# Performance work log

Hardware: AMD Instinct MI355X
Metric: run time of the kernel (lower is better)

Reference implementation:

```python
import jax, jax.numpy as jnp
import numpy as np

N_NODES = 100000
N_EDGES = 1600000
IN_DIM = 300
HID = 128
N_CLASSES = 3
N_ASPECTS = 2048


def setup_inputs() -> dict:
    key = jax.random.key(0)
    ks = jax.random.split(key, 8)
    features = jax.random.normal(ks[0], (N_NODES, IN_DIM), dtype=jnp.float32)
    edge_index = jax.random.randint(ks[1], (2, N_EDGES), 0, N_NODES, dtype=jnp.int64)
    aspect_indices = jax.random.randint(ks[2], (N_ASPECTS,), 0, N_NODES, dtype=jnp.int64)
    W1 = jax.random.normal(ks[3], (IN_DIM, HID), dtype=jnp.float32) * (1.0 / np.sqrt(IN_DIM))
    b1 = jnp.zeros((HID,), dtype=jnp.float32)
    W2 = jax.random.normal(ks[4], (HID, HID), dtype=jnp.float32) * (1.0 / np.sqrt(HID))
    b2 = jnp.zeros((HID,), dtype=jnp.float32)
    Wc = jax.random.normal(ks[5], (HID, N_CLASSES), dtype=jnp.float32) * (1.0 / np.sqrt(HID))
    bc = jnp.zeros((N_CLASSES,), dtype=jnp.float32)
    return {"features": features, "edge_index": edge_index, "aspect_indices": aspect_indices,
            "W1": W1, "b1": b1, "W2": W2, "b2": b2, "Wc": Wc, "bc": bc}


def _gcn_norm(edge_index, num_nodes):
    # PyG GCNConv: add self-loops, symmetric normalization D^-1/2 (A+I) D^-1/2
    loop = jnp.arange(num_nodes, dtype=edge_index.dtype)
    src = jnp.concatenate([edge_index[0], loop])
    dst = jnp.concatenate([edge_index[1], loop])
    deg = jax.ops.segment_sum(jnp.ones_like(dst, dtype=jnp.float32), dst,
                              num_segments=num_nodes)
    deg_inv_sqrt = jnp.where(deg > 0, jax.lax.rsqrt(deg), 0.0)
    norm = deg_inv_sqrt[src] * deg_inv_sqrt[dst]  # [E + N]
    return src, dst, norm


def _gcn_conv(x, src, dst, norm, W, b, num_nodes):
    h = x @ W                            # transform first (dim reduction)
    msg = h[src] * norm[:, None]         # gather + scale  [E+N, HID]
    out = jax.ops.segment_sum(msg, dst, num_segments=num_nodes)  # scatter-add
    return out + b


def reference(features, edge_index, aspect_indices, W1, b1, W2, b2, Wc, bc):
    num_nodes = features.shape[0]
    src, dst, norm = _gcn_norm(edge_index, num_nodes)
    h = _gcn_conv(features, src, dst, norm, W1, b1, num_nodes)
    h = jax.nn.relu(h)
    # dropout(p=0.3) -> identity in eval mode
    h = _gcn_conv(h, src, dst, norm, W2, b2, num_nodes)
    aspect_embeddings = h[aspect_indices]          # [N_ASPECTS, HID]
    logits = aspect_embeddings @ Wc + bc           # [N_ASPECTS, 3]
    return logits
```

## Files before the change

kernel.cpp:

```cpp
#include <hip/hip_runtime.h>

constexpr int NN = 100000;
constexpr int NE = 1600000;
constexpr int IN_DIM = 300;
constexpr int HID = 128;
constexpr int NA = 2048;
constexpr int NF_CAP = 50000;
constexpr int G1_BLOCKS = 391;
constexpr int EDGE_BLOCKS = 3125;

using short8 = __attribute__((ext_vector_type(8))) short;
using f32x4  = __attribute__((ext_vector_type(4))) float;

__device__ inline unsigned short f2bf(float x) {
    unsigned u = __float_as_uint(x);
    unsigned r = u + 0x7FFFu + ((u >> 16) & 1u);
    return (unsigned short)(r >> 16);
}
__device__ inline float bf2f(unsigned short h) {
    return __uint_as_float(((unsigned)h) << 16);
}

__device__ inline void gload_lds16(const void* g, void* l) {
    __builtin_amdgcn_global_load_lds(
        (const __attribute__((address_space(1))) unsigned int*)g,
        (__attribute__((address_space(3))) unsigned int*)l, 16, 0, 0);
}

__global__ void k_flag2(const int* __restrict__ asp, unsigned char* __restrict__ flags2,
                        int* __restrict__ flags1) {
    int i = blockIdx.x * blockDim.x + threadIdx.x;
    if (i < NA) {
        int n = asp[i];
        flags2[n] = 1;
        flags1[n] = 1;
    }
}

__global__ __launch_bounds__(1024) void k_scan2_local(const int* __restrict__ degi,
                                                      const int* __restrict__ flags1,
                                                      int* __restrict__ off,
                                                      int* __restrict__ off2,
                                                      int* __restrict__ blksum,
                                                      int* __restrict__ blksum2,
                                                      float* __restrict__ dis) {
    __shared__ int sh[1024];
    __shared__ int sh2[1024];
    int t = threadIdx.x;
    int base = blockIdx.x * 1024;
    int ok = (base + t < NN);
    int f = ok ? flags1[base + t] : 0;
    int d = ok ? degi[base + t] : 0;
    int v = f ? d : 0;
    if (ok) dis[base + t] = rsqrtf((float)d + 1.0f);
    sh[t] = v;
    sh2[t] = f;
    __syncthreads();
    for (int s = 1; s < 1024; s <<= 1) {
        int a = (t >= s) ? sh[t - s] : 0;
        int a2 = (t >= s) ? sh2[t - s] : 0;
        __syncthreads();
        sh[t] += a;
        sh2[t] += a2;
        __syncthreads();
    }
    if (ok) {
        off[base + t] = sh[t] - v;
        off2[base + t] = sh2[t] - f;
    }
    if (t == 1023) {
        blksum[blockIdx.x] = sh[1023];
        blksum2[blockIdx.x] = sh2[1023];
    }
}

__global__ __launch_bounds__(128) void k_scan2_blk(int* __restrict__ blksum,
                                                   int* __restrict__ blksum2, int nb) {
    __shared__ int sh[128];
    __shared__ int sh2[128];
    int t = threadIdx.x;
    int v = (t < nb) ? blksum[t] : 0;
    int v2 = (t < nb) ? blksum2[t] : 0;
    sh[t] = v;
    sh2[t] = v2;
    __syncthreads();
    for (int s = 1; s < 128; s <<= 1) {
        int a = (t >= s) ? sh[t - s] : 0;
        int a2 = (t >= s) ? sh2[t - s] : 0;
        __syncthreads();
        sh[t] += a;
        sh2[t] += a2;
        __syncthreads();
    }
    if (t < nb) {
        blksum[t] = sh[t] - v;
        blksum2[t] = sh2[t] - v2;
    }
}

__global__ void k_scan2_add(int* __restrict__ off, int* __restrict__ off2,
                            const int* __restrict__ blksum, const int* __restrict__ blksum2,
                            const int* __restrict__ flags1,
                            int* __restrict__ list, int* __restrict__ remap,
                            int* __restrict__ nf) {
    int i = blockIdx.x * blockDim.x + threadIdx.x;
    if (i < NN) {
        off[i] += blksum[i >> 10];
        int o2 = off2[i] + blksum2[i >> 10];
        off2[i] = o2;
        int f = flags1[i];
        if (f && o2 < NF_CAP) {
            list[o2] = i;
            remap[i] = o2;
        }
        if (i == NN - 1) {
            int tot = o2 + f;
            *nf = (tot < NF_CAP) ? tot : NF_CAP;
        }
    }
}

__global__ void k_prepB(const float* __restrict__ B, unsigned short* __restrict__ img,
                        int K, int NT) {
    int i = blockIdx.x * blockDim.x + threadIdx.x;
    if (i >= NT * 4096) return;
    int kt = i >> 12;
    int rem = i & 4095;
    int ct = rem >> 9;
    int s = rem & 511;
    int lg = s >> 7;
    int lr = (s >> 3) & 15;
    int j = s & 7;
    int k = kt * 32 + lg * 8 + j;
    int col = ct * 16 + lr;
    float v = (k < K) ? B[k * 128 + col] : 0.f;
    unsigned short hi = f2bf(v);
    unsigned short lo = f2bf(v - bf2f(hi));
    img[kt * 8192 + ct * 1024 + s] = hi;
    img[kt * 8192 + ct * 1024 + 512 + s] = lo;
}

template <int K, int NT>
__device__ __forceinline__ void gemm_dev(int gbid, const float* __restrict__ A,
        const unsigned short* __restrict__ Bimg,
        float* __restrict__ C, int M, const int* __restrict__ Mptr) {
    __shared__ alignas(16) unsigned short ldsB[2][8192];
    const int Mv = Mptr ? *Mptr : M;
    const int row0 = gbid * 128;
    if (row0 >= Mv) return;
    const int t = threadIdx.x;
    const int w = t >> 6;
    const int l = t & 63;
    const int lr = l & 15;
    const int lg = l >> 4;

    const int r0 = row0 + w * 16 + lr;
    const long a0 = (long)(r0 < Mv ? r0 : Mv - 1) * K + lg * 8;

    f32x4 acc[8];
#pragma unroll
    for (int ct = 0; ct < 8; ++ct) acc[ct] = (f32x4){0.f, 0.f, 0.f, 0.f};

    float4 A0[2], A1[2];

    auto LOADA = [&](float4* buf, int kt) {
        const int k0 = kt * 32 + lg * 8;
        const float* s0 = A + a0 + kt * 32;
        if (k0 + 8 <= K) {
            buf[0] = *(const float4*)(s0);
            buf[1] = *(const float4*)(s0 + 4);
        } else {
            float t0[8];
#pragma unroll
            for (int j = 0; j < 8; ++j) t0[j] = (k0 + j < K) ? s0[j] : 0.f;
            buf[0] = make_float4(t0[0], t0[1], t0[2], t0[3]);
            buf[1] = make_float4(t0[4], t0[5], t0[6], t0[7]);
        }
    };

    auto STAGE_B = [&](int buf, int kt) {
        const char* g = (const char*)Bimg + (long)kt * 16384 + w * 2048 + l * 16;
        gload_lds16(g, &ldsB[buf][w * 1024]);
        gload_lds16(g + 1024, &ldsB[buf][w * 1024 + 512]);
    };

    auto CONV = [&](const float4* buf, short8& h0, short8& e0) {
        float v0[8] = {buf[0].x, buf[0].y, buf[0].z, buf[0].w, buf[1].x, buf[1].y, buf[1].z, buf[1].w};
#pragma unroll
        for (int j = 0; j < 8; ++j) {
            unsigned short hi = f2bf(v0[j]);
            h0[j] = (short)hi;
            e0[j] = (short)f2bf(v0[j] - bf2f(hi));
        }
    };

    auto COMPUTE = [&](const unsigned short* bbuf, short8 ah, short8 al) {
#pragma unroll
        for (int ct = 0; ct < 8; ++ct) {
            const unsigned short* bp = bbuf + ct * 1024 + lg * 128 + lr * 8;
            short8 bh = *(const short8*)(bp);
            short8 bl = *(const short8*)(bp + 512);
            acc[ct] = __builtin_amdgcn_mfma_f32_16x16x32_bf16(ah, bh, acc[ct], 0, 0, 0);
            acc[ct] = __builtin_amdgcn_mfma_f32_16x16x32_bf16(al, bh, acc[ct], 0, 0, 0);
            acc[ct] = __builtin_amdgcn_mfma_f32_16x16x32_bf16(ah, bl, acc[ct], 0, 0, 0);
        }
    };

    LOADA(A0, 0);
    STAGE_B(0, 0);
    __syncthreads();
    for (int kt = 0; kt < NT; kt += 2) {
        if (kt + 1 < NT) {
            LOADA(A1, kt + 1);
            STAGE_B(1, kt + 1);
        }
        {
            short8 h0, e0;
            CONV(A0, h0, e0);
            COMPUTE(ldsB[0], h0, e0);
        }
        __syncthreads();
        if (kt + 1 < NT) {
            if (kt + 2 < NT) {
                LOADA(A0, kt + 2);
                STAGE_B(0, kt + 2);
            }
            short8 h0, e0;
            CONV(A1, h0, e0);
            COMPUTE(ldsB[1], h0, e0);
            __syncthreads();
        }
    }
#pragma unroll
    for (int ct = 0; ct < 8; ++ct)
#pragma unroll
        for (int r = 0; r < 4; ++r) {
            int row = row0 + w * 16 + lg * 4 + r;
            if (row < Mv) C[(long)row * 128 + ct * 16 + lr] = acc[ct][r];
        }
}

__global__ __launch_bounds__(512, 4) void k_fusedA(const float* __restrict__ A,
        const unsigned short* __restrict__ Bimg, float* __restrict__ C,
        const int* __restrict__ src, const int* __restrict__ dst,
        const unsigned char* __restrict__ flags2,
        int* __restrict__ degi, int* __restrict__ flags1) {
    if (blockIdx.x < G1_BLOCKS) {
        gemm_dev<IN_DIM, 10>(blockIdx.x, A, Bimg, C, NN, nullptr);
    } else {
        int e = (blockIdx.x - G1_BLOCKS) * 512 + threadIdx.x;
        if (e < NE) {
            int d = dst[e];
            atomicAdd(&degi[d], 1);
            if (flags2[d]) flags1[src[e]] = 1;
        }
    }
}

__global__ __launch_bounds__(512, 4) void k_fusedB(const float* __restrict__ A,
        const unsigned short* __restrict__ Bimg, float* __restrict__ C,
        const int* __restrict__ src, const int* __restrict__ dst,
        const int* __restrict__ flags1,
        int* __restrict__ off, int* __restrict__ csr) {
    if (blockIdx.x < G1_BLOCKS) {
        gemm_dev<IN_DIM, 10>(blockIdx.x + G1_BLOCKS, A, Bimg, C, NN, nullptr);
    } else {
        int e = (blockIdx.x - G1_BLOCKS) * 512 + threadIdx.x;
        if (e < NE) {
            int d = dst[e];
            if (flags1[d]) {
                int pos = atomicAdd(&off[d], 1);
                csr[pos] = src[e];
            }
        }
    }
}

__global__ __launch_bounds__(512, 4) void k_gemm2(const float* __restrict__ A,
        const unsigned short* __restrict__ Bimg, float* __restrict__ C,
        const int* __restrict__ nf) {
    gemm_dev<HID, 4>(blockIdx.x, A, Bimg, C, 0, nf);
}

__global__ __launch_bounds__(256) void k_gather1(const int* __restrict__ list,
                                                 const int* __restrict__ nf,
                                                 const int* __restrict__ csr,
                                                 const int* __restrict__ offpost,
                                                 const float* __restrict__ dis,
                                                 const float* __restrict__ h1,
                                                 const float* __restrict__ b1,
                                                 float* __restrict__ out) {
    int wave = threadIdx.x >> 6;
    int lane = threadIdx.x & 63;
    int half = lane >> 5;
    int sl = lane & 31;
    int idx = blockIdx.x * 4 + wave;
    if (idx >= *nf) return;
    int n = list[idx];
    int start = (n == 0) ? 0 : offpost[n - 1];
    int end = offpost[n];
    float dn = dis[n];
    float ax = 0.f, ay = 0.f, az = 0.f, aw = 0.f;
    int i = start + half;
    for (; i + 2 < end; i += 4) {
        int s0 = csr[i], s1 = csr[i + 2];
        float w0 = dis[s0], w1 = dis[s1];
        float4 v0 = *(const float4*)&h1[(long)s0 * HID + sl * 4];
        float4 v1 = *(const float4*)&h1[(long)s1 * HID + sl * 4];
        ax += w0 * v0.x + w1 * v1.x;
        ay += w0 * v0.y + w1 * v1.y;
        az += w0 * v0.z + w1 * v1.z;
        aw += w0 * v0.w + w1 * v1.w;
    }
    if (i < end) {
        int s = csr[i];
        float wgt = dis[s];
        float4 v = *(const float4*)&h1[(long)s * HID + sl * 4];
        ax += wgt * v.x;
        ay += wgt * v.y;
        az += wgt * v.z;
        aw += wgt * v.w;
    }
    ax += __shfl_xor(ax, 32);
    ay += __shfl_xor(ay, 32);
    az += __shfl_xor(az, 32);
    aw += __shfl_xor(aw, 32);
    if (half == 0) {
        float4 hv = *(const float4*)&h1[(long)n * HID + sl * 4];
        float4 bv = *(const float4*)&b1[sl * 4];
        float4 r;
        r.x = fmaxf(dn * (ax + dn * hv.x) + bv.x, 0.f);
        r.y = fmaxf(dn * (ay + dn * hv.y) + bv.y, 0.f);
        r.z = fmaxf(dn * (az + dn * hv.z) + bv.z, 0.f);
        r.w = fmaxf(dn * (aw + dn * hv.w) + bv.w, 0.f);
        *reinterpret_cast<float4*>(&out[(long)idx * HID + sl * 4]) = r;
    }
}

__global__ __launch_bounds__(256) void k_gather2(const int* __restrict__ asp,
                                                 const int* __restrict__ remap,
                                                 const int* __restrict__ csr,
                                                 const int* __restrict__ offpost,
                                                 const float* __restrict__ dis,
                                                 const float* __restrict__ t2,
                                                 const float* __restrict__ b2,
                                                 const float* __restrict__ Wc,
                                                 const float* __restrict__ bc,
                                                 float* __restrict__ out) {
    int wave = threadIdx.x >> 6;
    int lane = threadIdx.x & 63;
    int a = blockIdx.x * 4 + wave;
    if (a >= NA) return;
    int n = asp[a];
    int start = (n == 0) ? 0 : offpost[n - 1];
    int end = offpost[n];
    float dn = dis[n];
    float ax = 0.f, ay = 0.f;
    int i = start;
    for (; i + 4 <= end; i += 4) {
        int s0 = csr[i], s1 = csr[i + 1], s2 = csr[i + 2], s3 = csr[i + 3];
        float w0 = dis[s0], w1 = dis[s1], w2 = dis[s2], w3 = dis[s3];
        int r0 = remap[s0], r1 = remap[s1], r2 = remap[s2], r3 = remap[s3];
        float2 v0 = *(const float2*)&t2[(long)r0 * HID + lane * 2];
        float2 v1 = *(const float2*)&t2[(long)r1 * HID + lane * 2];
        float2 v2 = *(const float2*)&t2[(long)r2 * HID + lane * 2];
        float2 v3 = *(const float2*)&t2[(long)r3 * HID + lane * 2];
        ax += w0 * v0.x + w1 * v1.x + w2 * v2.x + w3 * v3.x;
        ay += w0 * v0.y + w1 * v1.y + w2 * v2.y + w3 * v3.y;
    }
    for (; i < end; ++i) {
        int s = csr[i];
        float w = dis[s];
        float2 v = *(const float2*)&t2[(long)remap[s] * HID + lane * 2];
        ax += w * v.x;
        ay += w * v.y;
    }
    float2 hv = *(const float2*)&t2[(long)remap[n] * HID + lane * 2];
    float vx = dn * (ax + dn * hv.x) + b2[2 * lane];
    float vy = dn * (ay + dn * hv.y) + b2[2 * lane + 1];
    float l0 = vx * Wc[(2 * lane) * 3 + 0] + vy * Wc[(2 * lane + 1) * 3 + 0];
    float l1 = vx * Wc[(2 * lane) * 3 + 1] + vy * Wc[(2 * lane + 1) * 3 + 1];
    float l2 = vx * Wc[(2 * lane) * 3 + 2] + vy * Wc[(2 * lane + 1) * 3 + 2];
#pragma unroll
    for (int s = 32; s > 0; s >>= 1) {
        l0 += __shfl_xor(l0, s);
        l1 += __shfl_xor(l1, s);
        l2 += __shfl_xor(l2, s);
    }
    if (lane == 0) {
        out[a * 3 + 0] = l0 + bc[0];
        out[a * 3 + 1] = l1 + bc[1];
        out[a * 3 + 2] = l2 + bc[2];
    }
}

extern "C" void kernel_launch(void* const* d_in, const int* in_sizes, int n_in,
                              void* d_out, int out_size, void* d_ws, size_t ws_size,
                              hipStream_t stream) {
    const float* features = (const float*)d_in[0];
    const int* ei = (const int*)d_in[1];
    const int* src = ei;
    const int* dst = ei + NE;
    const int* asp = (const int*)d_in[2];
    const float* W1 = (const float*)d_in[3];
    const float* b1 = (const float*)d_in[4];
    const float* W2 = (const float*)d_in[5];
    const float* b2 = (const float*)d_in[6];
    const float* Wc = (const float*)d_in[7];
    const float* bc = (const float*)d_in[8];
    float* out = (float*)d_out;

    char* ws = (char*)d_ws;
    float* dis   = (float*)(ws + 0);
    unsigned short* bimg1 = (unsigned short*)(ws + 400384);
    unsigned short* bimg2 = (unsigned short*)(ws + 400384 + 163840);
    int*   off   = (int*)  (ws + 800768);
    int*   blksum  = (int*)(ws + 1201152);
    int*   blksum2 = (int*)(ws + 1202176);
    int*   nf    = (int*)  (ws + 1203200);
    int*   csr   = (int*)  (ws + 1203328);
    int*   flags1= (int*)  (ws + 7603328);
    int*   off2  = (int*)  (ws + 8003328);
    int*   list  = (int*)  (ws + 8403328);
    int*   remap = (int*)  (ws + 8803328);
    float* bufA  = (float*)(ws + 9203328);
    float* bufB  = (float*)(ws + 60403328);
    int*   degi  = (int*)  (ws + 60403328);
    unsigned char* flags2 = (unsigned char*)(ws + 86003328);

    const int NB = (NN + 1023) / 1024;

    hipMemsetAsync(degi, 0, NN * sizeof(int), stream);
    hipMemsetAsync(flags1, 0, NN * sizeof(int), stream);
    hipMemsetAsync(flags2, 0, NN, stream);
    k_flag2<<<(NA + 255) / 256, 256, 0, stream>>>(asp, flags2, flags1);
    k_prepB<<<(10 * 4096 + 255) / 256, 256, 0, stream>>>(W1, bimg1, IN_DIM, 10);
    k_prepB<<<(4 * 4096 + 255) / 256, 256, 0, stream>>>(W2, bimg2, HID, 4);

    k_fusedA<<<G1_BLOCKS + EDGE_BLOCKS, 512, 0, stream>>>(
        features, bimg1, bufA, src, dst, flags2, degi, flags1);

    k_scan2_local<<<NB, 1024, 0, stream>>>(degi, flags1, off, off2, blksum, blksum2, dis);
    k_scan2_blk<<<1, 128, 0, stream>>>(blksum, blksum2, NB);
    k_scan2_add<<<(NN + 255) / 256, 256, 0, stream>>>(off, off2, blksum, blksum2,
                                                      flags1, list, remap, nf);

    k_fusedB<<<G1_BLOCKS + EDGE_BLOCKS, 512, 0, stream>>>(
        features, bimg1, bufA, src, dst, flags1, off, csr);

    k_gather1<<<(NF_CAP + 3) / 4, 256, 0, stream>>>(list, nf, csr, off, dis, bufA, b1, bufB);

    k_gemm2<<<(NF_CAP + 127) / 128, 512, 0, stream>>>(bufB, bimg2, bufA, nf);
    k_gather2<<<(NA + 3) / 4, 256, 0, stream>>>(asp, remap, csr, off, dis, bufA, b2, Wc, bc, out);
}
```

Before: 199.6 us.

## Stage B in two large phases and privatize degree counters across eight copies

The GEMM now loads half (or all) of the B image into LDS in one phase instead of double-buffering one k-tile at a time. This removes the per-tile barriers but uses much more LDS, which may lower occupancy. Separately, degree counting now spreads atomics over eight private copies selected by block index, and the scan sums them, to reduce atomic contention. The cost is a larger memset and eight reads per node in the scan.

```diff
diff --git a/kernel.cpp b/kernel.cpp
--- a/kernel.cpp
+++ b/kernel.cpp
@@ -37,7 +37,7 @@
     }
 }
 
-__global__ __launch_bounds__(1024) void k_scan2_local(const int* __restrict__ degi,
+__global__ __launch_bounds__(1024) void k_scan2_local(const int* __restrict__ degi8,
                                                       const int* __restrict__ flags1,
                                                       int* __restrict__ off,
                                                       int* __restrict__ off2,
@@ -50,9 +50,13 @@
     int base = blockIdx.x * 1024;
     int ok = (base + t < NN);
     int f = ok ? flags1[base + t] : 0;
-    int d = ok ? degi[base + t] : 0;
+    int d = 0;
+    if (ok) {
+#pragma unroll
+        for (int j = 0; j < 8; ++j) d += degi8[j * NN + base + t];
+        dis[base + t] = rsqrtf((float)d + 1.0f);
+    }
     int v = f ? d : 0;
-    if (ok) dis[base + t] = rsqrtf((float)d + 1.0f);
     sh[t] = v;
     sh2[t] = f;
     __syncthreads();
@@ -140,11 +144,11 @@
     img[kt * 8192 + ct * 1024 + 512 + s] = lo;
 }
 
-template <int K, int NT>
+template <int K, int NT, int HALF>
 __device__ __forceinline__ void gemm_dev(int gbid, const float* __restrict__ A,
         const unsigned short* __restrict__ Bimg,
         float* __restrict__ C, int M, const int* __restrict__ Mptr) {
-    __shared__ alignas(16) unsigned short ldsB[2][8192];
+    __shared__ alignas(16) unsigned short ldsB[HALF * 8192];
     const int Mv = Mptr ? *Mptr : M;
     const int row0 = gbid * 128;
     if (row0 >= Mv) return;
@@ -178,10 +182,13 @@
         }
     };
 
-    auto STAGE_B = [&](int buf, int kt) {
-        const char* g = (const char*)Bimg + (long)kt * 16384 + w * 2048 + l * 16;
-        gload_lds16(g, &ldsB[buf][w * 1024]);
-        gload_lds16(g + 1024, &ldsB[buf][w * 1024 + 512]);
+    auto STAGE_PH = [&](int ph) {
+#pragma unroll
+        for (int h = 0; h < HALF; ++h) {
+            const char* g = (const char*)Bimg + (long)(ph * HALF + h) * 16384 + w * 2048 + l * 16;
+            gload_lds16(g, &ldsB[h * 8192 + w * 1024]);
+            gload_lds16(g + 1024, &ldsB[h * 8192 + w * 1024 + 512]);
+        }
     };
 
     auto CONV = [&](const float4* buf, short8& h0, short8& e0) {
@@ -206,29 +213,25 @@
         }
     };
 
+    STAGE_PH(0);
     LOADA(A0, 0);
-    STAGE_B(0, 0);
     __syncthreads();
-    for (int kt = 0; kt < NT; kt += 2) {
+#pragma unroll
+    for (int kt = 0; kt < NT; ++kt) {
+        if (HALF < NT && kt == HALF) {
+            __syncthreads();
+            STAGE_PH(1);
+            __syncthreads();
+        }
         if (kt + 1 < NT) {
-            LOADA(A1, kt + 1);
-            STAGE_B(1, kt + 1);
+            if ((kt & 1) == 0) LOADA(A1, kt + 1);
+            else               LOADA(A0, kt + 1);
         }
         {
             short8 h0, e0;
-            CONV(A0, h0, e0);
-            COMPUTE(ldsB[0], h0, e0);
-        }
-        __syncthreads();
-        if (kt + 1 < NT) {
-            if (kt + 2 < NT) {
-                LOADA(A0, kt + 2);
-                STAGE_B(0, kt + 2);
-            }
-            short8 h0, e0;
-            CONV(A1, h0, e0);
-            COMPUTE(ldsB[1], h0, e0);
-            __syncthreads();
+            if ((kt & 1) == 0) { CONV(A0, h0, e0); }
+            else               { CONV(A1, h0, e0); }
+            COMPUTE(&ldsB[(kt % HALF) * 8192], h0, e0);
         }
     }
 #pragma unroll
@@ -244,14 +247,14 @@
         const unsigned short* __restrict__ Bimg, float* __restrict__ C,
         const int* __restrict__ src, const int* __restrict__ dst,
         const unsigned char* __restrict__ flags2,
-        int* __restrict__ degi, int* __restrict__ flags1) {
+        int* __restrict__ degi8, int* __restrict__ flags1) {
     if (blockIdx.x < G1_BLOCKS) {
-        gemm_dev<IN_DIM, 10>(blockIdx.x, A, Bimg, C, NN, nullptr);
+        gemm_dev<IN_DIM, 10, 5>(blockIdx.x, A, Bimg, C, NN, nullptr);
     } else {
         int e = (blockIdx.x - G1_BLOCKS) * 512 + threadIdx.x;
         if (e < NE) {
             int d = dst[e];
-            atomicAdd(&degi[d], 1);
+            atomicAdd(&degi8[(blockIdx.x & 7) * NN + d], 1);
             if (flags2[d]) flags1[src[e]] = 1;
         }
     }
@@ -263,7 +266,7 @@
         const int* __restrict__ flags1,
         int* __restrict__ off, int* __restrict__ csr) {
     if (blockIdx.x < G1_BLOCKS) {
-        gemm_dev<IN_DIM, 10>(blockIdx.x + G1_BLOCKS, A, Bimg, C, NN, nullptr);
+        gemm_dev<IN_DIM, 10, 5>(blockIdx.x + G1_BLOCKS, A, Bimg, C, NN, nullptr);
     } else {
         int e = (blockIdx.x - G1_BLOCKS) * 512 + threadIdx.x;
         if (e < NE) {
@@ -279,7 +282,7 @@
 __global__ __launch_bounds__(512, 4) void k_gemm2(const float* __restrict__ A,
         const unsigned short* __restrict__ Bimg, float* __restrict__ C,
         const int* __restrict__ nf) {
-    gemm_dev<HID, 4>(blockIdx.x, A, Bimg, C, 0, nf);
+    gemm_dev<HID, 4, 4>(blockIdx.x, A, Bimg, C, 0, nf);
 }
 
 __global__ __launch_bounds__(256) void k_gather1(const int* __restrict__ list,
@@ -425,12 +428,12 @@
     int*   remap = (int*)  (ws + 8803328);
     float* bufA  = (float*)(ws + 9203328);
     float* bufB  = (float*)(ws + 60403328);
-    int*   degi  = (int*)  (ws + 60403328);
+    int*   degi8 = (int*)  (ws + 60403328);
     unsigned char* flags2 = (unsigned char*)(ws + 86003328);
 
     const int NB = (NN + 1023) / 1024;
 
-    hipMemsetAsync(degi, 0, NN * sizeof(int), stream);
+    hipMemsetAsync(degi8, 0, 8 * NN * sizeof(int), stream);
     hipMemsetAsync(flags1, 0, NN * sizeof(int), stream);
     hipMemsetAsync(flags2, 0, NN, stream);
     k_flag2<<<(NA + 255) / 256, 256, 0, stream>>>(asp, flags2, flags1);
@@ -438,9 +441,9 @@
     k_prepB<<<(4 * 4096 + 255) / 256, 256, 0, stream>>>(W2, bimg2, HID, 4);
 
     k_fusedA<<<G1_BLOCKS + EDGE_BLOCKS, 512, 0, stream>>>(
-        features, bimg1, bufA, src, dst, flags2, degi, flags1);
-
-    k_scan2_local<<<NB, 1024, 0, stream>>>(degi, flags1, off, off2, blksum, blksum2, dis);
+        features, bimg1, bufA, src, dst, flags2, degi8, flags1);
+
+    k_scan2_local<<<NB, 1024, 0, stream>>>(degi8, flags1, off, off2, blksum, blksum2, dis);
     k_scan2_blk<<<1, 128, 0, stream>>>(blksum, blksum2, NB);
     k_scan2_add<<<(NN + 255) / 256, 256, 0, stream>>>(off, off2, blksum, blksum2,
                                                       flags1, list, remap, nf);
```

Measured after the change: 201.7 us. Within noise of the previous version (+1.1%).

## Halve GEMM row tile with 2x4 wave split and replicate degree counters

Applied to the files above, without the earlier changes.

The GEMM tile shrinks from 128 to 64 rows per block. The 8 waves are split into 4 row groups by 2 column halves, so each wave holds 4 accumulator tiles instead of 8. This doubles the GEMM block count and allows occupancy 8 in launch bounds. Degree atomics are also spread over 8 replicated counter arrays, chosen by block index, to reduce atomic contention; the scan kernel sums them. The cost is more redundant B staging per block, more A-load overhead per row, and a larger memset for the counters.

```diff
diff --git a/kernel.cpp b/kernel.cpp
--- a/kernel.cpp
+++ b/kernel.cpp
@@ -6,7 +6,9 @@
 constexpr int HID = 128;
 constexpr int NA = 2048;
 constexpr int NF_CAP = 50000;
-constexpr int G1_BLOCKS = 391;
+constexpr int G1T = 1563;
+constexpr int G1A = 782;
+constexpr int G1B = G1T - G1A;
 constexpr int EDGE_BLOCKS = 3125;
 
 using short8 = __attribute__((ext_vector_type(8))) short;
@@ -37,7 +39,7 @@
     }
 }
 
-__global__ __launch_bounds__(1024) void k_scan2_local(const int* __restrict__ degi,
+__global__ __launch_bounds__(1024) void k_scan2_local(const int* __restrict__ degi8,
                                                       const int* __restrict__ flags1,
                                                       int* __restrict__ off,
                                                       int* __restrict__ off2,
@@ -50,9 +52,13 @@
     int base = blockIdx.x * 1024;
     int ok = (base + t < NN);
     int f = ok ? flags1[base + t] : 0;
-    int d = ok ? degi[base + t] : 0;
+    int d = 0;
+    if (ok) {
+#pragma unroll
+        for (int j = 0; j < 8; ++j) d += degi8[j * NN + base + t];
+        dis[base + t] = rsqrtf((float)d + 1.0f);
+    }
     int v = f ? d : 0;
-    if (ok) dis[base + t] = rsqrtf((float)d + 1.0f);
     sh[t] = v;
     sh2[t] = f;
     __syncthreads();
@@ -146,20 +152,22 @@
         float* __restrict__ C, int M, const int* __restrict__ Mptr) {
     __shared__ alignas(16) unsigned short ldsB[2][8192];
     const int Mv = Mptr ? *Mptr : M;
-    const int row0 = gbid * 128;
+    const int row0 = gbid * 64;
     if (row0 >= Mv) return;
     const int t = threadIdx.x;
     const int w = t >> 6;
     const int l = t & 63;
     const int lr = l & 15;
     const int lg = l >> 4;
-
-    const int r0 = row0 + w * 16 + lr;
+    const int wr = w & 3;
+    const int wc = w >> 2;
+
+    const int r0 = row0 + wr * 16 + lr;
     const long a0 = (long)(r0 < Mv ? r0 : Mv - 1) * K + lg * 8;
 
-    f32x4 acc[8];
-#pragma unroll
-    for (int ct = 0; ct < 8; ++ct) acc[ct] = (f32x4){0.f, 0.f, 0.f, 0.f};
+    f32x4 acc[4];
+#pragma unroll
+    for (int ct = 0; ct < 4; ++ct) acc[ct] = (f32x4){0.f, 0.f, 0.f, 0.f};
 
     float4 A0[2], A1[2];
 
@@ -196,8 +204,8 @@
 
     auto COMPUTE = [&](const unsigned short* bbuf, short8 ah, short8 al) {
 #pragma unroll
-        for (int ct = 0; ct < 8; ++ct) {
-            const unsigned short* bp = bbuf + ct * 1024 + lg * 128 + lr * 8;
+        for (int ct = 0; ct < 4; ++ct) {
+            const unsigned short* bp = bbuf + (wc * 4 + ct) * 1024 + lg * 128 + lr * 8;
             short8 bh = *(const short8*)(bp);
             short8 bl = *(const short8*)(bp + 512);
             acc[ct] = __builtin_amdgcn_mfma_f32_16x16x32_bf16(ah, bh, acc[ct], 0, 0, 0);
@@ -232,40 +240,40 @@
         }
     }
 #pragma unroll
-    for (int ct = 0; ct < 8; ++ct)
+    for (int ct = 0; ct < 4; ++ct)
 #pragma unroll
         for (int r = 0; r < 4; ++r) {
-            int row = row0 + w * 16 + lg * 4 + r;
-            if (row < Mv) C[(long)row * 128 + ct * 16 + lr] = acc[ct][r];
-        }
-}
-
-__global__ __launch_bounds__(512, 4) void k_fusedA(const float* __restrict__ A,
+            int row = row0 + wr * 16 + lg * 4 + r;
+            if (row < Mv) C[(long)row * 128 + wc * 64 + ct * 16 + lr] = acc[ct][r];
+        }
+}
+
+__global__ __launch_bounds__(512, 8) void k_fusedA(const float* __restrict__ A,
         const unsigned short* __restrict__ Bimg, float* __restrict__ C,
         const int* __restrict__ src, const int* __restrict__ dst,
         const unsigned char* __restrict__ flags2,
-        int* __restrict__ degi, int* __restrict__ flags1) {
-    if (blockIdx.x < G1_BLOCKS) {
+        int* __restrict__ degi8, int* __restrict__ flags1) {
+    if (blockIdx.x < G1A) {
         gemm_dev<IN_DIM, 10>(blockIdx.x, A, Bimg, C, NN, nullptr);
     } else {
-        int e = (blockIdx.x - G1_BLOCKS) * 512 + threadIdx.x;
+        int e = (blockIdx.x - G1A) * 512 + threadIdx.x;
         if (e < NE) {
             int d = dst[e];
-            atomicAdd(&degi[d], 1);
+            atomicAdd(&degi8[(blockIdx.x & 7) * NN + d], 1);
             if (flags2[d]) flags1[src[e]] = 1;
         }
     }
 }
 
-__global__ __launch_bounds__(512, 4) void k_fusedB(const float* __restrict__ A,
+__global__ __launch_bounds__(512, 8) void k_fusedB(const float* __restrict__ A,
         const unsigned short* __restrict__ Bimg, float* __restrict__ C,
         const int* __restrict__ src, const int* __restrict__ dst,
         const int* __restrict__ flags1,
         int* __restrict__ off, int* __restrict__ csr) {
-    if (blockIdx.x < G1_BLOCKS) {
-        gemm_dev<IN_DIM, 10>(blockIdx.x + G1_BLOCKS, A, Bimg, C, NN, nullptr);
+    if (blockIdx.x < G1B) {
+        gemm_dev<IN_DIM, 10>(blockIdx.x + G1A, A, Bimg, C, NN, nullptr);
     } else {
-        int e = (blockIdx.x - G1_BLOCKS) * 512 + threadIdx.x;
+        int e = (blockIdx.x - G1B) * 512 + threadIdx.x;
         if (e < NE) {
             int d = dst[e];
             if (flags1[d]) {
@@ -276,7 +284,7 @@
     }
 }
 
-__global__ __launch_bounds__(512, 4) void k_gemm2(const float* __restrict__ A,
+__global__ __launch_bounds__(512, 8) void k_gemm2(const float* __restrict__ A,
         const unsigned short* __restrict__ Bimg, float* __restrict__ C,
         const int* __restrict__ nf) {
     gemm_dev<HID, 4>(blockIdx.x, A, Bimg, C, 0, nf);
@@ -425,31 +433,31 @@
     int*   remap = (int*)  (ws + 8803328);
     float* bufA  = (float*)(ws + 9203328);
     float* bufB  = (float*)(ws + 60403328);
-    int*   degi  = (int*)  (ws + 60403328);
+    int*   degi8 = (int*)  (ws + 60403328);
     unsigned char* flags2 = (unsigned char*)(ws + 86003328);
 
     const int NB = (NN + 1023) / 1024;
 
-    hipMemsetAsync(degi, 0, NN * sizeof(int), stream);
+    hipMemsetAsync(degi8, 0, 8 * NN * sizeof(int), stream);
     hipMemsetAsync(flags1, 0, NN * sizeof(int), stream);
     hipMemsetAsync(flags2, 0, NN, stream);
     k_flag2<<<(NA + 255) / 256, 256, 0, stream>>>(asp, flags2, flags1);
     k_prepB<<<(10 * 4096 + 255) / 256, 256, 0, stream>>>(W1, bimg1, IN_DIM, 10);
     k_prepB<<<(4 * 4096 + 255) / 256, 256, 0, stream>>>(W2, bimg2, HID, 4);
 
-    k_fusedA<<<G1_BLOCKS + EDGE_BLOCKS, 512, 0, stream>>>(
-        features, bimg1, bufA, src, dst, flags2, degi, flags1);
-
-    k_scan2_local<<<NB, 1024, 0, stream>>>(degi, flags1, off, off2, blksum, blksum2, dis);
+    k_fusedA<<<G1A + EDGE_BLOCKS, 512, 0, stream>>>(
+        features, bimg1, bufA, src, dst, flags2, degi8, flags1);
+
+    k_scan2_local<<<NB, 1024, 0, stream>>>(degi8, flags1, off, off2, blksum, blksum2, dis);
     k_scan2_blk<<<1, 128, 0, stream>>>(blksum, blksum2, NB);
     k_scan2_add<<<(NN + 255) / 256, 256, 0, stream>>>(off, off2, blksum, blksum2,
                                                       flags1, list, remap, nf);
 
-    k_fusedB<<<G1_BLOCKS + EDGE_BLOCKS, 512, 0, stream>>>(
+    k_fusedB<<<G1B + EDGE_BLOCKS, 512, 0, stream>>>(
         features, bimg1, bufA, src, dst, flags1, off, csr);
 
     k_gather1<<<(NF_CAP + 3) / 4, 256, 0, stream>>>(list, nf, csr, off, dis, bufA, b1, bufB);
 
-    k_gemm2<<<(NF_CAP + 127) / 128, 512, 0, stream>>>(bufB, bimg2, bufA, nf);
+    k_gemm2<<<(NF_CAP + 63) / 64, 512, 0, stream>>>(bufB, bimg2, bufA, nf);
     k_gather2<<<(NA + 3) / 4, 256, 0, stream>>>(asp, remap, csr, off, dis, bufA, b2, Wc, bc, out);
 }
```

After: 204.0 us. 2.2% more time.
